# Optimization experiments

Measured on AMD Instinct MI355X. Metric: run time of the kernel, lower is better.

The kernel has to match this reference:

```python
import jax, jax.numpy as jnp
import numpy as np

NSAMPLE = 64
RADIUS = 0.08
EPS = 1e-5
B, N, M, C = 4, 16384, 1024, 256


def ball_query(xyz, new_xyz, radius, nsample):
    """xyz [B,N,3], new_xyz [B,M,3] -> idx [B,M,nsample] int32.
    Picks first `nsample` points within `radius` of each query (in point order),
    padding with the first found index (0 if none), matching pointnet2 CUDA op."""
    b, n = xyz.shape[0], xyz.shape[1]
    m = new_xyz.shape[1]
    # squared distances via norms + matmul (avoids [B,M,N,3] intermediate)
    d2 = (jnp.sum(new_xyz * new_xyz, -1)[:, :, None]
          + jnp.sum(xyz * xyz, -1)[:, None, :]
          - 2.0 * jnp.einsum('bmc,bnc->bmn', new_xyz, xyz))  # [B,M,N]
    mask = d2 < radius * radius
    rank = jnp.cumsum(mask.astype(jnp.int32), axis=-1) - 1   # slot of each valid point
    valid = mask & (rank < nsample)
    slots = jnp.where(valid, rank, nsample)                  # invalid -> dump slot
    n_idx = jnp.broadcast_to(jnp.arange(n, dtype=jnp.int32), (b, m, n))
    b_idx = jnp.arange(b)[:, None, None]
    m_idx = jnp.arange(m)[None, :, None]
    idx = jnp.zeros((b, m, nsample + 1), jnp.int32)
    idx = idx.at[b_idx, m_idx, slots].set(n_idx)[..., :nsample]
    cnt = jnp.sum(mask, axis=-1)                             # [B,M] neighbors found
    pad = jnp.arange(nsample)[None, None, :] >= cnt[:, :, None]
    idx = jnp.where(pad, idx[:, :, :1], idx)                 # pad with first index
    return idx


def _mlp_layer(x, W, bias, gamma, beta, mu, var):
    # 1x1 conv (pointwise) + BatchNorm (eval, running stats) + ReLU, channels-last
    y = jnp.einsum('bmsc,oc->bmso', x, W) + bias
    y = (y - mu) * (gamma * jax.lax.rsqrt(var + EPS)) + beta
    return jax.nn.relu(y)


def reference(seed_xyz_fps, seed_xyz_graspable, seed_features_graspable,
              W1, b1, g1, be1, m1, v1, W2, b2, g2, be2, m2, v2):
    idx = ball_query(seed_xyz_fps, seed_xyz_graspable, RADIUS, NSAMPLE)  # [B,M,S]
    # gather + relative coordinates (use_xyz=True, normalize_xyz=False)
    gxyz = jax.vmap(lambda p, i: p[i])(seed_xyz_fps, idx)                # [B,M,S,3]
    gxyz = gxyz - seed_xyz_graspable[:, :, None, :]
    feats = jnp.swapaxes(seed_features_graspable, 1, 2)                  # [B,N,C]
    gfeat = jax.vmap(lambda f, i: f[i])(feats, idx)                      # [B,M,S,C]
    x = jnp.concatenate([gxyz, gfeat], axis=-1)                          # [B,M,S,3+C]
    x = _mlp_layer(x, W1, b1, g1, be1, m1, v1)                           # [B,M,S,256]
    x = _mlp_layer(x, W2, b2, g2, be2, m2, v2)                           # [B,M,S,256]
    x = jnp.max(x, axis=2)                                               # [B,M,256]
    return jnp.swapaxes(x, 1, 2)                                         # [B,256,M]


def setup_inputs() -> dict:
    key = jax.random.key(0)
    ks = jax.random.split(key, 16)
    return {
        'seed_xyz_fps': jax.random.uniform(ks[0], (B, N, 3), jnp.float32),
        'seed_xyz_graspable': jax.random.uniform(ks[1], (B, M, 3), jnp.float32),
        'seed_features_graspable': jax.random.normal(ks[2], (B, C, N), jnp.float32),
        'W1': jax.random.normal(ks[3], (256, 3 + C), jnp.float32) * 0.05,
        'b1': jax.random.normal(ks[4], (256,), jnp.float32) * 0.05,
        'g1': jax.random.uniform(ks[5], (256,), jnp.float32, 0.5, 1.5),
        'be1': jax.random.normal(ks[6], (256,), jnp.float32) * 0.05,
        'm1': jax.random.normal(ks[7], (256,), jnp.float32) * 0.1,
        'v1': jax.random.uniform(ks[8], (256,), jnp.float32, 0.5, 1.5),
        'W2': jax.random.normal(ks[9], (256, 256), jnp.float32) * 0.05,
        'b2': jax.random.normal(ks[10], (256,), jnp.float32) * 0.05,
        'g2': jax.random.uniform(ks[11], (256,), jnp.float32, 0.5, 1.5),
        'be2': jax.random.normal(ks[12], (256,), jnp.float32) * 0.05,
        'm2': jax.random.normal(ks[13], (256,), jnp.float32) * 0.1,
        'v2': jax.random.uniform(ks[14], (256,), jnp.float32, 0.5, 1.5),
    }
```

## Files before the change

### kernel.cpp

```cpp
#include <hip/hip_runtime.h>
#include <stdint.h>

typedef __bf16 bf16x8 __attribute__((ext_vector_type(8)));
typedef float f32x4 __attribute__((ext_vector_type(4)));

#define NSAMPLE 64
static constexpr int Bb = 4, Nn = 16384, Mm = 1024, Cc = 256;
static constexpr int K1P = 288;

__device__ __forceinline__ unsigned short f2bf(float f) {
  unsigned int u = __builtin_bit_cast(unsigned int, f);
  u = u + 0x7fffu + ((u >> 16) & 1u);
  return (unsigned short)(u >> 16);
}

__device__ __forceinline__ void gload_lds16(const void* g, void* lds) {
  __builtin_amdgcn_global_load_lds(
      (const __attribute__((address_space(1))) uint32_t*)g,
      (__attribute__((address_space(3))) uint32_t*)lds, 16, 0, 0);
}

__global__ void helpers_kernel(const float* __restrict__ xyz,
                               const float* __restrict__ new_xyz,
                               const float* __restrict__ feats,
                               const float* __restrict__ W1, const float* __restrict__ b1,
                               const float* __restrict__ g1, const float* __restrict__ be1,
                               const float* __restrict__ m1, const float* __restrict__ v1,
                               const float* __restrict__ W2, const float* __restrict__ b2,
                               const float* __restrict__ g2, const float* __restrict__ be2,
                               const float* __restrict__ m2, const float* __restrict__ v2,
                               unsigned short* __restrict__ W1b, float* __restrict__ b1e,
                               unsigned short* __restrict__ W2b, float* __restrict__ b2e,
                               unsigned short* __restrict__ featsT,
                               int* __restrict__ idx) {
  __shared__ float tile[64][65];
  __shared__ int wl[4][64];
  __shared__ int wcnt[4];
  int bx = blockIdx.x;
  int t = threadIdx.x;
  if (bx < 4096) {
    const float r2 = (float)(0.08 * 0.08);
    int bm = bx;
    int lane = t & 63, w = t >> 6;
    int b = bm >> 10;
    float qx = new_xyz[bm * 3], qy = new_xyz[bm * 3 + 1], qz = new_xyz[bm * 3 + 2];
    float qq = __fadd_rn(__fadd_rn(__fmul_rn(qx, qx), __fmul_rn(qy, qy)), __fmul_rn(qz, qz));
    const float* P = xyz + ((size_t)b * Nn + w * 4096) * 3;
    int cnt = 0;
    for (int n0 = 0; n0 < 4096; n0 += 64) {
      const float* pp = P + (n0 + lane) * 3;
      float x = pp[0], y = pp[1], z = pp[2];
      float p2 = __fadd_rn(__fadd_rn(__fmul_rn(x, x), __fmul_rn(y, y)), __fmul_rn(z, z));
      float dt = __fadd_rn(__fadd_rn(__fmul_rn(qx, x), __fmul_rn(qy, y)), __fmul_rn(qz, z));
      float d2 = __fsub_rn(__fadd_rn(qq, p2), __fmul_rn(2.f, dt));
      bool valid = d2 < r2;
      unsigned long long mask = __ballot(valid);
      if (mask) {
        if (valid) {
          int pos = cnt + __popcll(mask & ((1ull << lane) - 1ull));
          if (pos < NSAMPLE) wl[w][pos] = w * 4096 + n0 + lane;
        }
        cnt += (int)__popcll(mask);
        if (cnt >= NSAMPLE) break;
      }
    }
    if (lane == 0) wcnt[w] = cnt;
    __syncthreads();
    if (t < NSAMPLE) {
      int c0 = wcnt[0], c1 = wcnt[1], c2 = wcnt[2], c3 = wcnt[3];
      int tot = c0 + c1 + c2 + c3;
      int cc = tot < NSAMPLE ? tot : NSAMPLE;
      int v;
      if (t < cc) {
        if (t < c0) v = wl[0][t];
        else if (t < c0 + c1) v = wl[1][t - c0];
        else if (t < c0 + c1 + c2) v = wl[2][t - c0 - c1];
        else v = wl[3][t - c0 - c1 - c2];
      } else {
        v = (c0 > 0) ? wl[0][0] : (c1 > 0) ? wl[1][0] : (c2 > 0) ? wl[2][0] : (c3 > 0) ? wl[3][0] : 0;
      }
      idx[(size_t)bm * NSAMPLE + t] = v;
    }
    return;
  }
  if (bx < 8192) {
    int fb = bx - 4096;
    int b = fb >> 10;
    int rem = fb & 1023;
    int nt = rem >> 2, ct = rem & 3;
    int tx = t & 63, ty = t >> 6;
    const float* src = feats + ((size_t)b * Cc + ct * 64) * Nn + nt * 64;
#pragma unroll
    for (int i = 0; i < 16; i++) {
      int c = i * 4 + ty;
      tile[c][tx] = src[(size_t)c * Nn + tx];
    }
    __syncthreads();
    unsigned short* dst = featsT + ((size_t)b * Nn + nt * 64) * Cc + ct * 64;
    int c4 = (t & 15) * 4, n0 = t >> 4;
#pragma unroll
    for (int i = 0; i < 4; i++) {
      int n = i * 16 + n0;
      ushort4 v;
      v.x = f2bf(tile[c4][n]);
      v.y = f2bf(tile[c4 + 1][n]);
      v.z = f2bf(tile[c4 + 2][n]);
      v.w = f2bf(tile[c4 + 3][n]);
      *(ushort4*)&dst[(size_t)n * Cc + c4] = v;
    }
    return;
  }
  int g = (bx - 8192) * 256 + t;
  if (g < 256 * K1P) {
    int o = g / K1P, k = g - o * K1P;
    float s = g1[o] / sqrtf(v1[o] + 1e-5f);
    float w = 0.f;
    if (k < 256) w = W1[o * 259 + 3 + k];
    else if (k < 259) w = W1[o * 259 + (k - 256)];
    W1b[g] = f2bf(w * s);
  }
  if (g < 256 * 256) {
    int o = g >> 8;
    float s = g2[o] / sqrtf(v2[o] + 1e-5f);
    W2b[g] = f2bf(W2[g] * s);
  }
  if (g < 256) {
    float s1 = g1[g] / sqrtf(v1[g] + 1e-5f);
    b1e[g] = s1 * (b1[g] - m1[g]) + be1[g];
    float s2 = g2[g] / sqrtf(v2[g] + 1e-5f);
    b2e[g] = s2 * (b2[g] - m2[g]) + be2[g];
  }
}

__global__ __launch_bounds__(256, 4) void fused_kernel(
    const unsigned short* __restrict__ featsT, const float* __restrict__ xyz,
    const float* __restrict__ new_xyz, const int* __restrict__ idx,
    const unsigned short* __restrict__ W1b, const float* __restrict__ b1e,
    const unsigned short* __restrict__ W2b, const float* __restrict__ b2e,
    float* __restrict__ out) {
  __shared__ unsigned short Xf[64 * 256];
  __shared__ unsigned short Xco[64 * 40];
  int t = threadIdx.x;
  int wave = t >> 6, lane = t & 63;
  int lr = lane & 15, kg = lane >> 4;
  int wcol = wave * 64;
  int bm = blockIdx.x;
  int b = bm >> 10;

  if (t < 64) {
    int ci = idx[(size_t)bm * NSAMPLE + t];
    const float* pp = xyz + ((size_t)b * Nn + ci) * 3;
    float px = pp[0], py = pp[1], pz = pp[2];
    unsigned int c01 = (unsigned int)f2bf(px - new_xyz[bm * 3])
                     | ((unsigned int)f2bf(py - new_xyz[bm * 3 + 1]) << 16);
    unsigned int c2 = (unsigned int)f2bf(pz - new_xyz[bm * 3 + 2]);
    uint4 v0 = make_uint4(c01, c2, 0u, 0u);
    uint4 z = make_uint4(0u, 0u, 0u, 0u);
    uint4* row = (uint4*)&Xco[t * 40];
    row[0] = v0; row[1] = z; row[2] = z; row[3] = z; row[4] = z;
  }
  {
    int idxr = idx[(size_t)bm * NSAMPLE + wave * 16 + (lane & 15)];
#pragma unroll
    for (int i = 0; i < 8; i++) {
      int j = wave * 8 + i;
      int iv = __shfl(idxr, 2 * i + (lane >> 5));
      int r7 = (2 * j + (lane >> 5)) & 7;
      int cg = (lane & 31) ^ r7;
      gload_lds16(featsT + ((size_t)b * Nn + iv) * Cc + cg * 8, &Xf[j * 512]);
    }
  }
  __syncthreads();

  f32x4 acc[4][4];
#pragma unroll
  for (int mi = 0; mi < 4; mi++)
#pragma unroll
    for (int ni = 0; ni < 4; ni++) acc[mi][ni] = (f32x4){0.f, 0.f, 0.f, 0.f};
  {
    bf16x8 w[2][4];
#pragma unroll
    for (int ni = 0; ni < 4; ni++)
      w[0][ni] = *(const bf16x8*)&W1b[(size_t)(wcol + ni * 16 + lr) * K1P + kg * 8];
#pragma unroll
    for (int kk = 0; kk < 9; kk++) {
      int cur = kk & 1, nxt = cur ^ 1;
      if (kk < 8) {
#pragma unroll
        for (int ni = 0; ni < 4; ni++)
          w[nxt][ni] =
              *(const bf16x8*)&W1b[(size_t)(wcol + ni * 16 + lr) * K1P + (kk + 1) * 32 + kg * 8];
      }
      bf16x8 a[4];
#pragma unroll
      for (int mi = 0; mi < 4; mi++) {
        int r = mi * 16 + lr;
        if (kk < 8) {
          int cs = ((kk * 4 + kg) ^ (r & 7)) * 8;
          a[mi] = *(const bf16x8*)&Xf[r * 256 + cs];
        } else {
          a[mi] = *(const bf16x8*)&Xco[r * 40 + kg * 8];
        }
      }
      __builtin_amdgcn_s_setprio(1);
#pragma unroll
      for (int mi = 0; mi < 4; mi++)
#pragma unroll
        for (int ni = 0; ni < 4; ni++)
          acc[mi][ni] =
              __builtin_amdgcn_mfma_f32_16x16x32_bf16(a[mi], w[cur][ni], acc[mi][ni], 0, 0, 0);
      __builtin_amdgcn_s_setprio(0);
    }
  }
  __syncthreads();

#pragma unroll
  for (int ni = 0; ni < 4; ni++) {
    int o = wcol + ni * 16 + lr;
    float bb = b1e[o];
#pragma unroll
    for (int mi = 0; mi < 4; mi++)
#pragma unroll
      for (int j = 0; j < 4; j++) {
        int r = mi * 16 + kg * 4 + j;
        float h = fmaxf(acc[mi][ni][j] + bb, 0.f);
        Xf[r * 256 + ((((o >> 3) ^ (r & 7)) << 3) + (o & 7))] = f2bf(h);
      }
  }
  __syncthreads();

#pragma unroll
  for (int mi = 0; mi < 4; mi++)
#pragma unroll
    for (int ni = 0; ni < 4; ni++) acc[mi][ni] = (f32x4){0.f, 0.f, 0.f, 0.f};
  {
    bf16x8 w[2][4];
#pragma unroll
    for (int ni = 0; ni < 4; ni++)
      w[0][ni] = *(const bf16x8*)&W2b[(size_t)(wcol + ni * 16 + lr) * 256 + kg * 8];
#pragma unroll
    for (int kk = 0; kk < 8; kk++) {
      int cur = kk & 1, nxt = cur ^ 1;
      if (kk < 7) {
#pragma unroll
        for (int ni = 0; ni < 4; ni++)
          w[nxt][ni] =
              *(const bf16x8*)&W2b[(size_t)(wcol + ni * 16 + lr) * 256 + (kk + 1) * 32 + kg * 8];
      }
      bf16x8 a[4];
#pragma unroll
      for (int mi = 0; mi < 4; mi++) {
        int r = mi * 16 + lr;
        int cs = ((kk * 4 + kg) ^ (r & 7)) * 8;
        a[mi] = *(const bf16x8*)&Xf[r * 256 + cs];
      }
      __builtin_amdgcn_s_setprio(1);
#pragma unroll
      for (int mi = 0; mi < 4; mi++)
#pragma unroll
        for (int ni = 0; ni < 4; ni++)
          acc[mi][ni] =
              __builtin_amdgcn_mfma_f32_16x16x32_bf16(a[mi], w[cur][ni], acc[mi][ni], 0, 0, 0);
      __builtin_amdgcn_s_setprio(0);
    }
  }
  {
    int m = bm & (Mm - 1);
#pragma unroll
    for (int ni = 0; ni < 4; ni++) {
      float bv = b2e[wcol + ni * 16 + lr];
      float v = 0.f;
#pragma unroll
      for (int mi = 0; mi < 4; mi++)
#pragma unroll
        for (int j = 0; j < 4; j++) v = fmaxf(v, acc[mi][ni][j] + bv);
      v = fmaxf(v, __shfl_xor(v, 16));
      v = fmaxf(v, __shfl_xor(v, 32));
      if (kg == 0)
        out[((size_t)b * 256 + wcol + ni * 16 + lr) * Mm + m] = v;
    }
  }
}

extern "C" void kernel_launch(void* const* d_in, const int* in_sizes, int n_in,
                              void* d_out, int out_size, void* d_ws, size_t ws_size,
                              hipStream_t stream) {
  (void)in_sizes; (void)n_in; (void)out_size; (void)ws_size;
  const float* xyz     = (const float*)d_in[0];
  const float* new_xyz = (const float*)d_in[1];
  const float* feats   = (const float*)d_in[2];
  const float* W1 = (const float*)d_in[3];
  const float* b1 = (const float*)d_in[4];
  const float* g1 = (const float*)d_in[5];
  const float* be1 = (const float*)d_in[6];
  const float* m1 = (const float*)d_in[7];
  const float* v1 = (const float*)d_in[8];
  const float* W2 = (const float*)d_in[9];
  const float* b2 = (const float*)d_in[10];
  const float* g2 = (const float*)d_in[11];
  const float* be2 = (const float*)d_in[12];
  const float* m2 = (const float*)d_in[13];
  const float* v2 = (const float*)d_in[14];
  float* out = (float*)d_out;

  char* ws = (char*)d_ws;
  unsigned short* W1b   = (unsigned short*)(ws + 0);
  unsigned short* W2b   = (unsigned short*)(ws + 147456);
  float*          b1e   = (float*)(ws + 278528);
  float*          b2e   = (float*)(ws + 279552);
  unsigned short* featsT= (unsigned short*)(ws + 280576);
  int*            idx   = (int*)(ws + 33835008);

  helpers_kernel<<<4096 + 4096 + 288, 256, 0, stream>>>(
      xyz, new_xyz, feats, W1, b1, g1, be1, m1, v1, W2, b2, g2, be2, m2, v2,
      W1b, b1e, W2b, b2e, featsT, idx);
  fused_kernel<<<Bb * Mm, 256, 0, stream>>>(featsT, xyz, new_xyz, idx,
                                            W1b, b1e, W2b, b2e, out);
}
```

Measured before the change: 173.4 us.

## Batch four ball-query queries per block to reuse point loads

The ball-query section of the helper kernel now handles four query points per block. Each loaded point coordinate and its squared norm are reused across all four queries, and each query's early exit is tracked separately. This cuts ball-query blocks from 4096 to 1024 and shares global loads of xyz, but each block now runs until the slowest of its four queries fills up, with more registers and LDS. The fused kernel also issues its feature gather before the coordinate setup and drops the s_setprio hints around the MFMA loops.

```diff
diff --git a/kernel.cpp b/kernel.cpp
--- a/kernel.cpp
+++ b/kernel.cpp
@@ -34,57 +34,76 @@
                                unsigned short* __restrict__ featsT,
                                int* __restrict__ idx) {
   __shared__ float tile[64][65];
-  __shared__ int wl[4][64];
-  __shared__ int wcnt[4];
+  __shared__ int wl[4][4][64];
+  __shared__ int wcnt[4][4];
   int bx = blockIdx.x;
   int t = threadIdx.x;
-  if (bx < 4096) {
+  if (bx < 1024) {
     const float r2 = (float)(0.08 * 0.08);
-    int bm = bx;
+    int bm0 = bx * 4;
     int lane = t & 63, w = t >> 6;
-    int b = bm >> 10;
-    float qx = new_xyz[bm * 3], qy = new_xyz[bm * 3 + 1], qz = new_xyz[bm * 3 + 2];
-    float qq = __fadd_rn(__fadd_rn(__fmul_rn(qx, qx), __fmul_rn(qy, qy)), __fmul_rn(qz, qz));
+    int b = bm0 >> 10;
+    float qx[4], qy[4], qz[4], qq[4];
+    int cnt[4];
+#pragma unroll
+    for (int qi = 0; qi < 4; qi++) {
+      qx[qi] = new_xyz[(bm0 + qi) * 3];
+      qy[qi] = new_xyz[(bm0 + qi) * 3 + 1];
+      qz[qi] = new_xyz[(bm0 + qi) * 3 + 2];
+      qq[qi] = __fadd_rn(__fadd_rn(__fmul_rn(qx[qi], qx[qi]), __fmul_rn(qy[qi], qy[qi])),
+                         __fmul_rn(qz[qi], qz[qi]));
+      cnt[qi] = 0;
+    }
     const float* P = xyz + ((size_t)b * Nn + w * 4096) * 3;
-    int cnt = 0;
     for (int n0 = 0; n0 < 4096; n0 += 64) {
       const float* pp = P + (n0 + lane) * 3;
       float x = pp[0], y = pp[1], z = pp[2];
       float p2 = __fadd_rn(__fadd_rn(__fmul_rn(x, x), __fmul_rn(y, y)), __fmul_rn(z, z));
-      float dt = __fadd_rn(__fadd_rn(__fmul_rn(qx, x), __fmul_rn(qy, y)), __fmul_rn(qz, z));
-      float d2 = __fsub_rn(__fadd_rn(qq, p2), __fmul_rn(2.f, dt));
-      bool valid = d2 < r2;
-      unsigned long long mask = __ballot(valid);
-      if (mask) {
-        if (valid) {
-          int pos = cnt + __popcll(mask & ((1ull << lane) - 1ull));
-          if (pos < NSAMPLE) wl[w][pos] = w * 4096 + n0 + lane;
+#pragma unroll
+      for (int qi = 0; qi < 4; qi++) {
+        if (cnt[qi] >= NSAMPLE) continue;
+        float dt = __fadd_rn(__fadd_rn(__fmul_rn(qx[qi], x), __fmul_rn(qy[qi], y)),
+                             __fmul_rn(qz[qi], z));
+        float d2 = __fsub_rn(__fadd_rn(qq[qi], p2), __fmul_rn(2.f, dt));
+        bool valid = d2 < r2;
+        unsigned long long mask = __ballot(valid);
+        if (mask) {
+          if (valid) {
+            int pos = cnt[qi] + __popcll(mask & ((1ull << lane) - 1ull));
+            if (pos < NSAMPLE) wl[qi][w][pos] = w * 4096 + n0 + lane;
+          }
+          cnt[qi] += (int)__popcll(mask);
         }
-        cnt += (int)__popcll(mask);
-        if (cnt >= NSAMPLE) break;
-      }
-    }
-    if (lane == 0) wcnt[w] = cnt;
+      }
+      if (cnt[0] >= NSAMPLE && cnt[1] >= NSAMPLE && cnt[2] >= NSAMPLE && cnt[3] >= NSAMPLE)
+        break;
+    }
+    if (lane == 0) {
+#pragma unroll
+      for (int qi = 0; qi < 4; qi++) wcnt[qi][w] = cnt[qi];
+    }
     __syncthreads();
-    if (t < NSAMPLE) {
-      int c0 = wcnt[0], c1 = wcnt[1], c2 = wcnt[2], c3 = wcnt[3];
+    {
+      int qi = t >> 6, s = t & 63;
+      int c0 = wcnt[qi][0], c1 = wcnt[qi][1], c2 = wcnt[qi][2], c3 = wcnt[qi][3];
       int tot = c0 + c1 + c2 + c3;
       int cc = tot < NSAMPLE ? tot : NSAMPLE;
       int v;
-      if (t < cc) {
-        if (t < c0) v = wl[0][t];
-        else if (t < c0 + c1) v = wl[1][t - c0];
-        else if (t < c0 + c1 + c2) v = wl[2][t - c0 - c1];
-        else v = wl[3][t - c0 - c1 - c2];
+      if (s < cc) {
+        if (s < c0) v = wl[qi][0][s];
+        else if (s < c0 + c1) v = wl[qi][1][s - c0];
+        else if (s < c0 + c1 + c2) v = wl[qi][2][s - c0 - c1];
+        else v = wl[qi][3][s - c0 - c1 - c2];
       } else {
-        v = (c0 > 0) ? wl[0][0] : (c1 > 0) ? wl[1][0] : (c2 > 0) ? wl[2][0] : (c3 > 0) ? wl[3][0] : 0;
-      }
-      idx[(size_t)bm * NSAMPLE + t] = v;
+        v = (c0 > 0) ? wl[qi][0][0] : (c1 > 0) ? wl[qi][1][0]
+          : (c2 > 0) ? wl[qi][2][0] : (c3 > 0) ? wl[qi][3][0] : 0;
+      }
+      idx[(size_t)(bm0 + qi) * NSAMPLE + s] = v;
     }
     return;
   }
-  if (bx < 8192) {
-    int fb = bx - 4096;
+  if (bx < 5120) {
+    int fb = bx - 1024;
     int b = fb >> 10;
     int rem = fb & 1023;
     int nt = rem >> 2, ct = rem & 3;
@@ -110,7 +129,7 @@
     }
     return;
   }
-  int g = (bx - 8192) * 256 + t;
+  int g = (bx - 5120) * 256 + t;
   if (g < 256 * K1P) {
     int o = g / K1P, k = g - o * K1P;
     float s = g1[o] / sqrtf(v1[o] + 1e-5f);
@@ -147,6 +166,17 @@
   int bm = blockIdx.x;
   int b = bm >> 10;
 
+  {
+    int idxr = idx[(size_t)bm * NSAMPLE + wave * 16 + (lane & 15)];
+#pragma unroll
+    for (int i = 0; i < 8; i++) {
+      int j = wave * 8 + i;
+      int iv = __shfl(idxr, 2 * i + (lane >> 5));
+      int r7 = (2 * j + (lane >> 5)) & 7;
+      int cg = (lane & 31) ^ r7;
+      gload_lds16(featsT + ((size_t)b * Nn + iv) * Cc + cg * 8, &Xf[j * 512]);
+    }
+  }
   if (t < 64) {
     int ci = idx[(size_t)bm * NSAMPLE + t];
     const float* pp = xyz + ((size_t)b * Nn + ci) * 3;
@@ -159,17 +189,6 @@
     uint4* row = (uint4*)&Xco[t * 40];
     row[0] = v0; row[1] = z; row[2] = z; row[3] = z; row[4] = z;
   }
-  {
-    int idxr = idx[(size_t)bm * NSAMPLE + wave * 16 + (lane & 15)];
-#pragma unroll
-    for (int i = 0; i < 8; i++) {
-      int j = wave * 8 + i;
-      int iv = __shfl(idxr, 2 * i + (lane >> 5));
-      int r7 = (2 * j + (lane >> 5)) & 7;
-      int cg = (lane & 31) ^ r7;
-      gload_lds16(featsT + ((size_t)b * Nn + iv) * Cc + cg * 8, &Xf[j * 512]);
-    }
-  }
   __syncthreads();
 
   f32x4 acc[4][4];
@@ -202,14 +221,12 @@
           a[mi] = *(const bf16x8*)&Xco[r * 40 + kg * 8];
         }
       }
-      __builtin_amdgcn_s_setprio(1);
 #pragma unroll
       for (int mi = 0; mi < 4; mi++)
 #pragma unroll
         for (int ni = 0; ni < 4; ni++)
           acc[mi][ni] =
               __builtin_amdgcn_mfma_f32_16x16x32_bf16(a[mi], w[cur][ni], acc[mi][ni], 0, 0, 0);
-      __builtin_amdgcn_s_setprio(0);
     }
   }
   __syncthreads();
@@ -254,14 +271,12 @@
         int cs = ((kk * 4 + kg) ^ (r & 7)) * 8;
         a[mi] = *(const bf16x8*)&Xf[r * 256 + cs];
       }
-      __builtin_amdgcn_s_setprio(1);
 #pragma unroll
       for (int mi = 0; mi < 4; mi++)
 #pragma unroll
         for (int ni = 0; ni < 4; ni++)
           acc[mi][ni] =
               __builtin_amdgcn_mfma_f32_16x16x32_bf16(a[mi], w[cur][ni], acc[mi][ni], 0, 0, 0);
-      __builtin_amdgcn_s_setprio(0);
     }
   }
   {
@@ -311,7 +326,7 @@
   unsigned short* featsT= (unsigned short*)(ws + 280576);
   int*            idx   = (int*)(ws + 33835008);
 
-  helpers_kernel<<<4096 + 4096 + 288, 256, 0, stream>>>(
+  helpers_kernel<<<1024 + 4096 + 288, 256, 0, stream>>>(
       xyz, new_xyz, feats, W1, b1, g1, be1, m1, v1, W2, b2, g2, be2, m2, v2,
       W1b, b1e, W2b, b2e, featsT, idx);
   fused_kernel<<<Bb * Mm, 256, 0, stream>>>(featsT, xyz, new_xyz, idx,
```

New measurement: 152.7 us. -11.9%, faster.
